# Performance work log

Measured on AMD Instinct MI355X. Metric: run time of the kernel, lower is better.

The kernel has to match this reference:

```python
import jax, jax.numpy as jnp
import numpy as np

D_MODEL, D_HIDDEN, N_EXPERTS, TOP_K = 1024, 2048, 8, 2


def setup_inputs() -> dict:
    key = jax.random.key(0)
    ks = jax.random.split(key, 8)
    s_in = 1.0 / np.sqrt(D_MODEL)
    s_hid = 1.0 / np.sqrt(D_HIDDEN)
    return {
        "x": jax.random.normal(ks[0], (1, 2048, D_MODEL), dtype=jnp.float32),
        # stacked expert weights, stored (in, out) so y = x @ W + b
        "W1": jax.random.normal(ks[1], (N_EXPERTS, D_MODEL, D_HIDDEN), dtype=jnp.float32) * s_in,
        "b1": jnp.zeros((N_EXPERTS, D_HIDDEN), dtype=jnp.float32),
        "W2": jax.random.normal(ks[2], (N_EXPERTS, D_MODEL, D_HIDDEN), dtype=jnp.float32) * s_in,
        "b2": jnp.zeros((N_EXPERTS, D_HIDDEN), dtype=jnp.float32),
        "Wo": jax.random.normal(ks[3], (N_EXPERTS, D_HIDDEN, D_MODEL), dtype=jnp.float32) * s_hid,
        "bo": jnp.zeros((N_EXPERTS, D_MODEL), dtype=jnp.float32),
        "Wr": jax.random.normal(ks[4], (D_MODEL, N_EXPERTS), dtype=jnp.float32) * s_in,
        "br": jnp.zeros((N_EXPERTS,), dtype=jnp.float32),
    }


def reference(x, W1, b1, W2, b2, Wo, bo, Wr, br):
    B, S, D = x.shape
    T = B * S
    xf = x.reshape(T, D)

    # router
    logits = xf @ Wr + br                      # [T, E]
    probs = jax.nn.softmax(logits, axis=-1)
    topk_probs, topk_idx = jax.lax.top_k(probs, TOP_K)  # [T, K]

    # combine weights: c[t, e] = sum_k topk_probs[t, k] * 1[topk_idx[t, k] == e]
    c = jnp.zeros((T, N_EXPERTS), dtype=xf.dtype)
    c = c.at[jnp.arange(T)[:, None], topk_idx].add(topk_probs)  # [T, E]

    # per-expert SwiGLU FFN applied densely, then masked-combined (same math
    # as the original gather/scatter loop since c[t,e]=0 for unrouted experts)
    h = jnp.einsum('td,edh->eth', xf, W1) + b1[:, None, :]   # [E, T, H]
    g = jnp.einsum('td,edh->eth', xf, W2) + b2[:, None, :]
    y = jnp.einsum('eth,ehd->etd', h * jax.nn.silu(g), Wo) + bo[:, None, :]
    out = jnp.einsum('etd,te->td', y, c).reshape(B, S, D)

    probs_mean = probs.mean(axis=0)
    lb_loss = (probs_mean * probs_mean).sum() * N_EXPERTS
    return out, lb_loss
```

## Files before the change

kernel.cpp:

```cpp
#include <hip/hip_runtime.h>
#include <hip/hip_bf16.h>

#define T_TOK 2048
#define DM 1024
#define DH 2048
#define NE 8
#define MT_MAX 40

using bf16x8 = __attribute__((ext_vector_type(8))) short;
using f32x4  = __attribute__((ext_vector_type(4))) float;

__device__ __forceinline__ unsigned short f2bf(float f) {
  union { float f; unsigned u; } v; v.f = f;
  unsigned r = v.u + 0x7FFFu + ((v.u >> 16) & 1u);
  return (unsigned short)(r >> 16);
}
__device__ __forceinline__ unsigned pk2(float a, float b) {
  return (unsigned)f2bf(a) | ((unsigned)f2bf(b) << 16);
}

#define GLOAD16(gsrc, ldst)                                                        \
  __builtin_amdgcn_global_load_lds(                                                \
      (const __attribute__((address_space(1))) unsigned int*)(gsrc),               \
      (__attribute__((address_space(3))) unsigned int*)(ldst), 16, 0, 0)

__global__ __launch_bounds__(256) void k_router(
    const float* __restrict__ x, const float* __restrict__ Wr, const float* __restrict__ br,
    int* __restrict__ cnt, int* __restrict__ idx, float* __restrict__ wgt,
    int* __restrict__ t2r, float* __restrict__ probs, unsigned short* __restrict__ xb)
{
  const int wave = threadIdx.x >> 6, l = threadIdx.x & 63;
  const int t = blockIdx.x * 4 + wave;
  float xv[16];
#pragma unroll
  for (int i = 0; i < 16; ++i) xv[i] = x[t*DM + l + 64*i];
#pragma unroll
  for (int i = 0; i < 16; ++i) xb[t*DM + l + 64*i] = f2bf(xv[i]);

  float acc[8] = {0.f,0.f,0.f,0.f,0.f,0.f,0.f,0.f};
#pragma unroll
  for (int i = 0; i < 16; ++i) {
    const float4* wp = (const float4*)&Wr[(size_t)(l + 64*i)*NE];
    float4 wa = wp[0], wb = wp[1];
    acc[0] += xv[i]*wa.x; acc[1] += xv[i]*wa.y; acc[2] += xv[i]*wa.z; acc[3] += xv[i]*wa.w;
    acc[4] += xv[i]*wb.x; acc[5] += xv[i]*wb.y; acc[6] += xv[i]*wb.z; acc[7] += xv[i]*wb.w;
  }
#pragma unroll
  for (int e = 0; e < 8; ++e) {
#pragma unroll
    for (int off = 32; off; off >>= 1) acc[e] += __shfl_xor(acc[e], off, 64);
    acc[e] += br[e];
  }
  float mx = acc[0];
#pragma unroll
  for (int e = 1; e < 8; ++e) mx = fmaxf(mx, acc[e]);
  float p[8], s = 0.f;
#pragma unroll
  for (int e = 0; e < 8; ++e) { p[e] = expf(acc[e] - mx); s += p[e]; }
  float inv = 1.f / s;
#pragma unroll
  for (int e = 0; e < 8; ++e) p[e] *= inv;

  int e0 = 0; float p0 = p[0];
#pragma unroll
  for (int e = 1; e < 8; ++e) if (p[e] > p0) { p0 = p[e]; e0 = e; }
  int e1 = -1; float p1 = -1.f;
#pragma unroll
  for (int e = 0; e < 8; ++e) { if (e == e0) continue; if (p[e] > p1) { p1 = p[e]; e1 = e; } }

  if (l == 0) {
#pragma unroll
    for (int e = 0; e < 8; ++e) probs[t*NE + e] = p[e];
    int pos0 = atomicAdd(&cnt[e0], 1);
    idx[e0*T_TOK + pos0] = t; wgt[e0*T_TOK + pos0] = p0;
    t2r[t*2 + 0] = e0*T_TOK + pos0;
    int pos1 = atomicAdd(&cnt[e1], 1);
    idx[e1*T_TOK + pos1] = t; wgt[e1*T_TOK + pos1] = p1;
    t2r[t*2 + 1] = e1*T_TOK + pos1;
  }
}

__global__ __launch_bounds__(256) void k_finalize(
    const int* __restrict__ cnt, int* __restrict__ rb,
    const float* __restrict__ probs, float* __restrict__ out,
    int* __restrict__ MTp, int* __restrict__ mtab)
{
  __shared__ float red[8][256];
  const int tid = threadIdx.x;
  float s[8] = {0.f,0.f,0.f,0.f,0.f,0.f,0.f,0.f};
  for (int t = tid; t < T_TOK; t += 256) {
#pragma unroll
    for (int e = 0; e < 8; ++e) s[e] += probs[t*NE + e];
  }
#pragma unroll
  for (int e = 0; e < 8; ++e) red[e][tid] = s[e];
  __syncthreads();
  for (int w = 128; w > 0; w >>= 1) {
    if (tid < w) {
#pragma unroll
      for (int e = 0; e < 8; ++e) red[e][tid] += red[e][tid + w];
    }
    __syncthreads();
  }
  if (tid == 0) {
    float lb = 0.f;
#pragma unroll
    for (int e = 0; e < 8; ++e) {
      float mean = red[e][0] * (1.f / T_TOK);
      lb += mean * mean;
    }
    out[2097152] = lb * NE;
    int r = 0, mc = 0;
#pragma unroll
    for (int e = 0; e < 8; ++e) {
      rb[e] = r; r += cnt[e];
      int nmt = (cnt[e] + 127) / 128;
      for (int j = 0; j < nmt; ++j) mtab[mc++] = (e << 16) | j;
    }
    *MTp = mc;
  }
}

__global__ __launch_bounds__(256) void k_convT(
    const float* __restrict__ in, unsigned short* __restrict__ outT,
    int R, int C, int nnt)
{
  const int e = blockIdx.z;
  const int r0 = blockIdx.y * 64, c0 = blockIdx.x * 64;
  __shared__ float t[64][65];
  const int tid = threadIdx.x;
  const int lr = tid >> 4, lc = (tid & 15) * 4;
#pragma unroll
  for (int i = 0; i < 4; ++i) {
    float4 v = *(const float4*)&in[((size_t)e*R + r0 + lr + i*16)*C + c0 + lc];
    t[lr + i*16][lc+0] = v.x; t[lr + i*16][lc+1] = v.y;
    t[lr + i*16][lc+2] = v.z; t[lr + i*16][lc+3] = v.w;
  }
  __syncthreads();
  const int oc = tid >> 3;
  const int od = (tid & 7) * 8;
  const size_t base2 = ((size_t)e*128 + (size_t)(r0 >> 6)*nnt + (c0 >> 8)) * 16384
                     + (size_t)(c0 & 255) * 64;
#pragma unroll
  for (int i = 0; i < 2; ++i) {
    int c = oc + i*32;
    uint4 v;
    v.x = pk2(t[od+0][c], t[od+1][c]);
    v.y = pk2(t[od+2][c], t[od+3][c]);
    v.z = pk2(t[od+4][c], t[od+5][c]);
    v.w = pk2(t[od+6][c], t[od+7][c]);
    *(uint4*)&outT[base2 + (size_t)c*64 + od] = v;
  }
}

#define TM1 128
#define TN1 64
#define BKK 64

__global__ __launch_bounds__(256) void k_ffn1b(
    const unsigned short* __restrict__ xb,
    const unsigned short* __restrict__ W1T, const float* __restrict__ b1,
    const unsigned short* __restrict__ W2T, const float* __restrict__ b2,
    const int* __restrict__ cnt, const int* __restrict__ rbp,
    const int* __restrict__ idx, unsigned short* __restrict__ act,
    const int* __restrict__ MTp, const int* __restrict__ mtab)
{
  const int mtg = blockIdx.y;
  if (mtg >= *MTp) return;
  const int code = mtab[mtg];
  const int e = code >> 16, mt = code & 0xffff;
  const int Me = cnt[e];
  const int m0 = mt * TM1;
  const int nt = blockIdx.x;
  const int n0 = nt * TN1;

  __shared__ __align__(16) unsigned short As[TM1*BKK];
  __shared__ __align__(16) unsigned short Bh[TN1*BKK];
  __shared__ __align__(16) unsigned short Bg[TN1*BKK];
  __shared__ int toks[TM1];

  const int tid = threadIdx.x;
  if (tid < TM1) toks[tid] = idx[e*T_TOK + min(m0 + tid, Me - 1)];
  __syncthreads();

  const int lane = tid & 63;
  const int wave = tid >> 6;
  const int wm = wave >> 1, wn = wave & 1;
  const int row16 = lane & 15, kg = lane >> 4;
  const int sl = lane & 7;
  const int lr = lane >> 3;

  const unsigned short* asrc[4];
#pragma unroll
  for (int i = 0; i < 4; ++i) {
    int r = (wave*4 + i)*8 + lr;
    asrc[i] = &xb[(size_t)toks[r]*DM + ((sl ^ (r & 7)) * 8)];
  }
  const unsigned short *bsrc1[2], *bsrc2[2];
  const int nt256 = n0 >> 8, nsub = n0 & 255;
#pragma unroll
  for (int j = 0; j < 2; ++j) {
    int r = (wave*2 + j)*8 + lr;
    size_t gb = ((size_t)e*128 + nt256)*16384 + (size_t)(nsub + r)*64 + ((sl ^ (r & 7)) * 8);
    bsrc1[j] = &W1T[gb]; bsrc2[j] = &W2T[gb];
  }

  f32x4 ah[4][2], ag[4][2];
#pragma unroll
  for (int i = 0; i < 4; ++i)
#pragma unroll
    for (int j = 0; j < 2; ++j) { ah[i][j] = 0.f; ag[i][j] = 0.f; }

  for (int k0 = 0; k0 < DM; k0 += BKK) {
    const size_t bko = (size_t)k0 * 2048;
#pragma unroll
    for (int i = 0; i < 4; ++i)
      GLOAD16(asrc[i] + k0, &As[(wave*4 + i)*512]);
#pragma unroll
    for (int j = 0; j < 2; ++j) {
      GLOAD16(bsrc1[j] + bko, &Bh[(wave*2 + j)*512]);
      GLOAD16(bsrc2[j] + bko, &Bg[(wave*2 + j)*512]);
    }
    __syncthreads();
#pragma unroll
    for (int ks = 0; ks < 2; ++ks) {
      const int kslot = ks*4 + kg;
      bf16x8 a[4], vbh[2], vbg[2];
#pragma unroll
      for (int mi = 0; mi < 4; ++mi) {
        int m = wm*64 + mi*16 + row16;
        a[mi] = *(const bf16x8*)&As[m*BKK + ((kslot ^ (m & 7)) * 8)];
      }
#pragma unroll
      for (int ni = 0; ni < 2; ++ni) {
        int n = wn*32 + ni*16 + row16;
        int off = n*BKK + ((kslot ^ (n & 7)) * 8);
        vbh[ni] = *(const bf16x8*)&Bh[off];
        vbg[ni] = *(const bf16x8*)&Bg[off];
      }
#pragma unroll
      for (int mi = 0; mi < 4; ++mi)
#pragma unroll
        for (int ni = 0; ni < 2; ++ni) {
          ah[mi][ni] = __builtin_amdgcn_mfma_f32_16x16x32_bf16(a[mi], vbh[ni], ah[mi][ni], 0, 0, 0);
          ag[mi][ni] = __builtin_amdgcn_mfma_f32_16x16x32_bf16(a[mi], vbg[ni], ag[mi][ni], 0, 0, 0);
        }
    }
    __syncthreads();
  }

  const int rb = rbp[e];
#pragma unroll
  for (int mi = 0; mi < 4; ++mi) {
#pragma unroll
    for (int i = 0; i < 4; ++i) {
      int rloc = wm*64 + mi*16 + (lane >> 4)*4 + i;
      int m = m0 + rloc;
      if (m < Me) {
#pragma unroll
        for (int ni = 0; ni < 2; ++ni) {
          int col = n0 + wn*32 + ni*16 + row16;
          float h = ah[mi][ni][i] + b1[e*DH + col];
          float g = ag[mi][ni][i] + b2[e*DH + col];
          float sg = g / (1.f + __expf(-g));
          act[(size_t)(rb + m)*DH + col] = f2bf(h * sg);
        }
      }
    }
  }
}

__global__ __launch_bounds__(256) void k_ffn2b(
    const unsigned short* __restrict__ act,
    const unsigned short* __restrict__ WoT, const float* __restrict__ bo,
    const int* __restrict__ cnt, const int* __restrict__ rbp,
    const int* __restrict__ idx, const float* __restrict__ wgt,
    float* __restrict__ out,
    const int* __restrict__ MTp, const int* __restrict__ mtab)
{
  const int mtg = blockIdx.y;
  if (mtg >= *MTp) return;
  const int code = mtab[mtg];
  const int e = code >> 16, mt = code & 0xffff;
  const int Me = cnt[e];
  const int m0 = mt * TM1;
  const int nt = blockIdx.x;
  const int n0 = nt * TN1;
  const int rb = rbp[e];

  __shared__ __align__(16) unsigned short As[TM1*BKK];
  __shared__ __align__(16) unsigned short Bs[TN1*BKK];
  __shared__ int   toks[TM1];
  __shared__ float wgts[TM1];

  const int tid = threadIdx.x;
  if (tid < TM1) {
    int p = min(m0 + tid, Me - 1);
    toks[tid] = idx[e*T_TOK + p];
    wgts[tid] = wgt[e*T_TOK + p];
  }

  const int lane = tid & 63;
  const int wave = tid >> 6;
  const int wm = wave >> 1, wn = wave & 1;
  const int row16 = lane & 15, kg = lane >> 4;
  const int sl = lane & 7;
  const int lr = lane >> 3;

  const unsigned short* asrc[4];
#pragma unroll
  for (int i = 0; i < 4; ++i) {
    int r = (wave*4 + i)*8 + lr;
    int grow = rb + min(m0 + r, Me - 1);
    asrc[i] = &act[(size_t)grow*DH + ((sl ^ (r & 7)) * 8)];
  }
  const unsigned short* bsrc[2];
  const int nt256 = n0 >> 8, nsub = n0 & 255;
#pragma unroll
  for (int j = 0; j < 2; ++j) {
    int r = (wave*2 + j)*8 + lr;
    size_t gb = ((size_t)e*128 + nt256)*16384 + (size_t)(nsub + r)*64 + ((sl ^ (r & 7)) * 8);
    bsrc[j] = &WoT[gb];
  }

  f32x4 acc[4][2];
#pragma unroll
  for (int i = 0; i < 4; ++i)
#pragma unroll
    for (int j = 0; j < 2; ++j) acc[i][j] = 0.f;

  for (int k0 = 0; k0 < DH; k0 += BKK) {
    const size_t bko = (size_t)k0 * 1024;
#pragma unroll
    for (int i = 0; i < 4; ++i)
      GLOAD16(asrc[i] + k0, &As[(wave*4 + i)*512]);
#pragma unroll
    for (int j = 0; j < 2; ++j)
      GLOAD16(bsrc[j] + bko, &Bs[(wave*2 + j)*512]);
    __syncthreads();
#pragma unroll
    for (int ks = 0; ks < 2; ++ks) {
      const int kslot = ks*4 + kg;
      bf16x8 a[4], b[2];
#pragma unroll
      for (int mi = 0; mi < 4; ++mi) {
        int m = wm*64 + mi*16 + row16;
        a[mi] = *(const bf16x8*)&As[m*BKK + ((kslot ^ (m & 7)) * 8)];
      }
#pragma unroll
      for (int ni = 0; ni < 2; ++ni) {
        int n = wn*32 + ni*16 + row16;
        b[ni] = *(const bf16x8*)&Bs[n*BKK + ((kslot ^ (n & 7)) * 8)];
      }
#pragma unroll
      for (int mi = 0; mi < 4; ++mi)
#pragma unroll
        for (int ni = 0; ni < 2; ++ni)
          acc[mi][ni] = __builtin_amdgcn_mfma_f32_16x16x32_bf16(a[mi], b[ni], acc[mi][ni], 0, 0, 0);
    }
    __syncthreads();
  }

#pragma unroll
  for (int mi = 0; mi < 4; ++mi) {
#pragma unroll
    for (int i = 0; i < 4; ++i) {
      int rloc = wm*64 + mi*16 + (lane >> 4)*4 + i;
      int m = m0 + rloc;
      if (m < Me) {
        const int t = toks[rloc];
        const float w = wgts[rloc];
#pragma unroll
        for (int ni = 0; ni < 2; ++ni) {
          int col = n0 + wn*32 + ni*16 + row16;
          float y = acc[mi][ni][i] + bo[e*DM + col];
          atomicAdd(&out[(size_t)t*DM + col], w * y);
        }
      }
    }
  }
}

extern "C" void kernel_launch(void* const* d_in, const int* in_sizes, int n_in,
                              void* d_out, int out_size, void* d_ws, size_t ws_size,
                              hipStream_t stream)
{
  const float* x  = (const float*)d_in[0];
  const float* W1 = (const float*)d_in[1];
  const float* b1 = (const float*)d_in[2];
  const float* W2 = (const float*)d_in[3];
  const float* b2 = (const float*)d_in[4];
  const float* Wo = (const float*)d_in[5];
  const float* bo = (const float*)d_in[6];
  const float* Wr = (const float*)d_in[7];
  const float* br = (const float*)d_in[8];
  float* out = (float*)d_out;

  char* ws = (char*)d_ws;
  int*   cnt   = (int*)(ws + 0);
  int*   rb    = (int*)(ws + 64);
  int*   MTp   = (int*)(ws + 128);
  int*   mtab  = (int*)(ws + 192);
  int*   t2r   = (int*)(ws + 4096);
  int*   idx   = (int*)(ws + 32*1024);
  float* wgt   = (float*)(ws + 96*1024);
  float* probs = (float*)(ws + 160*1024);
  unsigned short* xb  = (unsigned short*)(ws + 256*1024);
  unsigned short* act = (unsigned short*)(ws + 5ull*1024*1024);
  unsigned short* W1T = (unsigned short*)(ws + 40ull*1024*1024);
  unsigned short* W2T = (unsigned short*)(ws + 72ull*1024*1024);
  unsigned short* WoT = (unsigned short*)(ws + 104ull*1024*1024);

  hipMemsetAsync(out, 0, (size_t)out_size * sizeof(float), stream);
  hipMemsetAsync(cnt, 0, NE * sizeof(int), stream);
  k_router<<<T_TOK/4, 256, 0, stream>>>(x, Wr, br, cnt, idx, wgt, t2r, probs, xb);
  k_finalize<<<1, 256, 0, stream>>>(cnt, rb, probs, out, MTp, mtab);
  k_convT<<<dim3(DH/64, DM/64, NE), 256, 0, stream>>>(W1, W1T, DM, DH, 8);
  k_convT<<<dim3(DH/64, DM/64, NE), 256, 0, stream>>>(W2, W2T, DM, DH, 8);
  k_convT<<<dim3(DM/64, DH/64, NE), 256, 0, stream>>>(Wo, WoT, DH, DM, 4);
  k_ffn1b<<<dim3(DH/TN1, MT_MAX), 256, 0, stream>>>(xb, W1T, b1, W2T, b2, cnt, rb, idx, act, MTp, mtab);
  k_ffn2b<<<dim3(DM/TN1, MT_MAX), 256, 0, stream>>>(act, WoT, bo, cnt, rb, idx, wgt, out, MTp, mtab);
}
```

Before: 223.5 us.

## Fuse router with weight conversion kernels and widen ffn2 N tile

```diff
diff --git a/kernel.cpp b/kernel.cpp
--- a/kernel.cpp
+++ b/kernel.cpp
@@ -24,59 +24,99 @@
       (const __attribute__((address_space(1))) unsigned int*)(gsrc),               \
       (__attribute__((address_space(3))) unsigned int*)(ldst), 16, 0, 0)
 
-__global__ __launch_bounds__(256) void k_router(
+__global__ __launch_bounds__(256) void k_rconv(
     const float* __restrict__ x, const float* __restrict__ Wr, const float* __restrict__ br,
     int* __restrict__ cnt, int* __restrict__ idx, float* __restrict__ wgt,
-    int* __restrict__ t2r, float* __restrict__ probs, unsigned short* __restrict__ xb)
+    float* __restrict__ probs, unsigned short* __restrict__ xb,
+    const float* __restrict__ W1, const float* __restrict__ W2, const float* __restrict__ Wo,
+    unsigned short* __restrict__ W1T, unsigned short* __restrict__ W2T,
+    unsigned short* __restrict__ WoT)
 {
-  const int wave = threadIdx.x >> 6, l = threadIdx.x & 63;
-  const int t = blockIdx.x * 4 + wave;
-  float xv[16];
-#pragma unroll
-  for (int i = 0; i < 16; ++i) xv[i] = x[t*DM + l + 64*i];
-#pragma unroll
-  for (int i = 0; i < 16; ++i) xb[t*DM + l + 64*i] = f2bf(xv[i]);
-
-  float acc[8] = {0.f,0.f,0.f,0.f,0.f,0.f,0.f,0.f};
-#pragma unroll
-  for (int i = 0; i < 16; ++i) {
-    const float4* wp = (const float4*)&Wr[(size_t)(l + 64*i)*NE];
-    float4 wa = wp[0], wb = wp[1];
-    acc[0] += xv[i]*wa.x; acc[1] += xv[i]*wa.y; acc[2] += xv[i]*wa.z; acc[3] += xv[i]*wa.w;
-    acc[4] += xv[i]*wb.x; acc[5] += xv[i]*wb.y; acc[6] += xv[i]*wb.z; acc[7] += xv[i]*wb.w;
-  }
-#pragma unroll
-  for (int e = 0; e < 8; ++e) {
-#pragma unroll
-    for (int off = 32; off; off >>= 1) acc[e] += __shfl_xor(acc[e], off, 64);
-    acc[e] += br[e];
-  }
-  float mx = acc[0];
-#pragma unroll
-  for (int e = 1; e < 8; ++e) mx = fmaxf(mx, acc[e]);
-  float p[8], s = 0.f;
-#pragma unroll
-  for (int e = 0; e < 8; ++e) { p[e] = expf(acc[e] - mx); s += p[e]; }
-  float inv = 1.f / s;
-#pragma unroll
-  for (int e = 0; e < 8; ++e) p[e] *= inv;
-
-  int e0 = 0; float p0 = p[0];
-#pragma unroll
-  for (int e = 1; e < 8; ++e) if (p[e] > p0) { p0 = p[e]; e0 = e; }
-  int e1 = -1; float p1 = -1.f;
-#pragma unroll
-  for (int e = 0; e < 8; ++e) { if (e == e0) continue; if (p[e] > p1) { p1 = p[e]; e1 = e; } }
-
-  if (l == 0) {
-#pragma unroll
-    for (int e = 0; e < 8; ++e) probs[t*NE + e] = p[e];
-    int pos0 = atomicAdd(&cnt[e0], 1);
-    idx[e0*T_TOK + pos0] = t; wgt[e0*T_TOK + pos0] = p0;
-    t2r[t*2 + 0] = e0*T_TOK + pos0;
-    int pos1 = atomicAdd(&cnt[e1], 1);
-    idx[e1*T_TOK + pos1] = t; wgt[e1*T_TOK + pos1] = p1;
-    t2r[t*2 + 1] = e1*T_TOK + pos1;
+  __shared__ float ts[64][65];
+  const int tid = threadIdx.x;
+
+  if (blockIdx.x < 512) {
+    const int wave = tid >> 6, l = tid & 63;
+    const int t = blockIdx.x * 4 + wave;
+    float xv[16];
+#pragma unroll
+    for (int i = 0; i < 16; ++i) xv[i] = x[t*DM + l + 64*i];
+#pragma unroll
+    for (int i = 0; i < 16; ++i) xb[t*DM + l + 64*i] = f2bf(xv[i]);
+
+    float acc[8] = {0.f,0.f,0.f,0.f,0.f,0.f,0.f,0.f};
+#pragma unroll
+    for (int i = 0; i < 16; ++i) {
+      const float4* wp = (const float4*)&Wr[(size_t)(l + 64*i)*NE];
+      float4 wa = wp[0], wb = wp[1];
+      acc[0] += xv[i]*wa.x; acc[1] += xv[i]*wa.y; acc[2] += xv[i]*wa.z; acc[3] += xv[i]*wa.w;
+      acc[4] += xv[i]*wb.x; acc[5] += xv[i]*wb.y; acc[6] += xv[i]*wb.z; acc[7] += xv[i]*wb.w;
+    }
+#pragma unroll
+    for (int e = 0; e < 8; ++e) {
+#pragma unroll
+      for (int off = 32; off; off >>= 1) acc[e] += __shfl_xor(acc[e], off, 64);
+      acc[e] += br[e];
+    }
+    float mx = acc[0];
+#pragma unroll
+    for (int e = 1; e < 8; ++e) mx = fmaxf(mx, acc[e]);
+    float p[8], s = 0.f;
+#pragma unroll
+    for (int e = 0; e < 8; ++e) { p[e] = expf(acc[e] - mx); s += p[e]; }
+    float inv = 1.f / s;
+#pragma unroll
+    for (int e = 0; e < 8; ++e) p[e] *= inv;
+
+    int e0 = 0; float p0 = p[0];
+#pragma unroll
+    for (int e = 1; e < 8; ++e) if (p[e] > p0) { p0 = p[e]; e0 = e; }
+    int e1 = -1; float p1 = -1.f;
+#pragma unroll
+    for (int e = 0; e < 8; ++e) { if (e == e0) continue; if (p[e] > p1) { p1 = p[e]; e1 = e; } }
+
+    if (l == 0) {
+#pragma unroll
+      for (int e = 0; e < 8; ++e) probs[t*NE + e] = p[e];
+      int pos0 = atomicAdd(&cnt[e0], 1);
+      idx[e0*T_TOK + pos0] = t; wgt[e0*T_TOK + pos0] = p0;
+      int pos1 = atomicAdd(&cnt[e1], 1);
+      idx[e1*T_TOK + pos1] = t; wgt[e1*T_TOK + pos1] = p1;
+    }
+    return;
+  }
+
+  int b = blockIdx.x - 512;
+  const float* in; unsigned short* outT; int R, C, nnt, csh;
+  if (b < 4096)      { in = W1; outT = W1T; R = DM; C = DH; nnt = 8; csh = 5; }
+  else if (b < 8192) { in = W2; outT = W2T; R = DM; C = DH; nnt = 8; csh = 5; b -= 4096; }
+  else               { in = Wo; outT = WoT; R = DH; C = DM; nnt = 4; csh = 4; b -= 8192; }
+  const int e  = b >> 9;
+  const int te = b & 511;
+  const int r0 = (te >> csh) << 6;
+  const int c0 = (te & ((1 << csh) - 1)) << 6;
+
+  const int lr = tid >> 4, lc = (tid & 15) * 4;
+#pragma unroll
+  for (int i = 0; i < 4; ++i) {
+    float4 v = *(const float4*)&in[((size_t)e*R + r0 + lr + i*16)*C + c0 + lc];
+    ts[lr + i*16][lc+0] = v.x; ts[lr + i*16][lc+1] = v.y;
+    ts[lr + i*16][lc+2] = v.z; ts[lr + i*16][lc+3] = v.w;
+  }
+  __syncthreads();
+  const int oc = tid >> 3;
+  const int od = (tid & 7) * 8;
+  const size_t base2 = ((size_t)e*128 + (size_t)(r0 >> 6)*nnt + (c0 >> 8)) * 16384
+                     + (size_t)(c0 & 255) * 64;
+#pragma unroll
+  for (int i = 0; i < 2; ++i) {
+    int c = oc + i*32;
+    uint4 v;
+    v.x = pk2(ts[od+0][c], ts[od+1][c]);
+    v.y = pk2(ts[od+2][c], ts[od+3][c]);
+    v.z = pk2(ts[od+4][c], ts[od+5][c]);
+    v.w = pk2(ts[od+6][c], ts[od+7][c]);
+    *(uint4*)&outT[base2 + (size_t)c*64 + od] = v;
   }
 }
 
@@ -118,38 +158,6 @@
       for (int j = 0; j < nmt; ++j) mtab[mc++] = (e << 16) | j;
     }
     *MTp = mc;
-  }
-}
-
-__global__ __launch_bounds__(256) void k_convT(
-    const float* __restrict__ in, unsigned short* __restrict__ outT,
-    int R, int C, int nnt)
-{
-  const int e = blockIdx.z;
-  const int r0 = blockIdx.y * 64, c0 = blockIdx.x * 64;
-  __shared__ float t[64][65];
-  const int tid = threadIdx.x;
-  const int lr = tid >> 4, lc = (tid & 15) * 4;
-#pragma unroll
-  for (int i = 0; i < 4; ++i) {
-    float4 v = *(const float4*)&in[((size_t)e*R + r0 + lr + i*16)*C + c0 + lc];
-    t[lr + i*16][lc+0] = v.x; t[lr + i*16][lc+1] = v.y;
-    t[lr + i*16][lc+2] = v.z; t[lr + i*16][lc+3] = v.w;
-  }
-  __syncthreads();
-  const int oc = tid >> 3;
-  const int od = (tid & 7) * 8;
-  const size_t base2 = ((size_t)e*128 + (size_t)(r0 >> 6)*nnt + (c0 >> 8)) * 16384
-                     + (size_t)(c0 & 255) * 64;
-#pragma unroll
-  for (int i = 0; i < 2; ++i) {
-    int c = oc + i*32;
-    uint4 v;
-    v.x = pk2(t[od+0][c], t[od+1][c]);
-    v.y = pk2(t[od+2][c], t[od+3][c]);
-    v.z = pk2(t[od+4][c], t[od+5][c]);
-    v.w = pk2(t[od+6][c], t[od+7][c]);
-    *(uint4*)&outT[base2 + (size_t)c*64 + od] = v;
   }
 }
 
@@ -270,6 +278,8 @@
   }
 }
 
+#define TN2 128
+
 __global__ __launch_bounds__(256) void k_ffn2b(
     const unsigned short* __restrict__ act,
     const unsigned short* __restrict__ WoT, const float* __restrict__ bo,
@@ -285,11 +295,11 @@
   const int Me = cnt[e];
   const int m0 = mt * TM1;
   const int nt = blockIdx.x;
-  const int n0 = nt * TN1;
+  const int n0 = nt * TN2;
   const int rb = rbp[e];
 
   __shared__ __align__(16) unsigned short As[TM1*BKK];
-  __shared__ __align__(16) unsigned short Bs[TN1*BKK];
+  __shared__ __align__(16) unsigned short Bs[TN2*BKK];
   __shared__ int   toks[TM1];
   __shared__ float wgts[TM1];
 
@@ -314,20 +324,20 @@
     int grow = rb + min(m0 + r, Me - 1);
     asrc[i] = &act[(size_t)grow*DH + ((sl ^ (r & 7)) * 8)];
   }
-  const unsigned short* bsrc[2];
+  const unsigned short* bsrc[4];
   const int nt256 = n0 >> 8, nsub = n0 & 255;
 #pragma unroll
-  for (int j = 0; j < 2; ++j) {
-    int r = (wave*2 + j)*8 + lr;
+  for (int j = 0; j < 4; ++j) {
+    int r = (wave*4 + j)*8 + lr;
     size_t gb = ((size_t)e*128 + nt256)*16384 + (size_t)(nsub + r)*64 + ((sl ^ (r & 7)) * 8);
     bsrc[j] = &WoT[gb];
   }
 
-  f32x4 acc[4][2];
+  f32x4 acc[4][4];
 #pragma unroll
   for (int i = 0; i < 4; ++i)
 #pragma unroll
-    for (int j = 0; j < 2; ++j) acc[i][j] = 0.f;
+    for (int j = 0; j < 4; ++j) acc[i][j] = 0.f;
 
   for (int k0 = 0; k0 < DH; k0 += BKK) {
     const size_t bko = (size_t)k0 * 1024;
@@ -335,27 +345,27 @@
     for (int i = 0; i < 4; ++i)
       GLOAD16(asrc[i] + k0, &As[(wave*4 + i)*512]);
 #pragma unroll
-    for (int j = 0; j < 2; ++j)
-      GLOAD16(bsrc[j] + bko, &Bs[(wave*2 + j)*512]);
+    for (int j = 0; j < 4; ++j)
+      GLOAD16(bsrc[j] + bko, &Bs[(wave*4 + j)*512]);
     __syncthreads();
 #pragma unroll
     for (int ks = 0; ks < 2; ++ks) {
       const int kslot = ks*4 + kg;
-      bf16x8 a[4], b[2];
+      bf16x8 a[4], b[4];
 #pragma unroll
       for (int mi = 0; mi < 4; ++mi) {
         int m = wm*64 + mi*16 + row16;
         a[mi] = *(const bf16x8*)&As[m*BKK + ((kslot ^ (m & 7)) * 8)];
       }
 #pragma unroll
-      for (int ni = 0; ni < 2; ++ni) {
-        int n = wn*32 + ni*16 + row16;
+      for (int ni = 0; ni < 4; ++ni) {
+        int n = wn*64 + ni*16 + row16;
         b[ni] = *(const bf16x8*)&Bs[n*BKK + ((kslot ^ (n & 7)) * 8)];
       }
 #pragma unroll
       for (int mi = 0; mi < 4; ++mi)
 #pragma unroll
-        for (int ni = 0; ni < 2; ++ni)
+        for (int ni = 0; ni < 4; ++ni)
           acc[mi][ni] = __builtin_amdgcn_mfma_f32_16x16x32_bf16(a[mi], b[ni], acc[mi][ni], 0, 0, 0);
     }
     __syncthreads();
@@ -371,8 +381,8 @@
         const int t = toks[rloc];
         const float w = wgts[rloc];
 #pragma unroll
-        for (int ni = 0; ni < 2; ++ni) {
-          int col = n0 + wn*32 + ni*16 + row16;
+        for (int ni = 0; ni < 4; ++ni) {
+          int col = n0 + wn*64 + ni*16 + row16;
           float y = acc[mi][ni][i] + bo[e*DM + col];
           atomicAdd(&out[(size_t)t*DM + col], w * y);
         }
@@ -401,7 +411,6 @@
   int*   rb    = (int*)(ws + 64);
   int*   MTp   = (int*)(ws + 128);
   int*   mtab  = (int*)(ws + 192);
-  int*   t2r   = (int*)(ws + 4096);
   int*   idx   = (int*)(ws + 32*1024);
   float* wgt   = (float*)(ws + 96*1024);
   float* probs = (float*)(ws + 160*1024);
@@ -413,11 +422,9 @@
 
   hipMemsetAsync(out, 0, (size_t)out_size * sizeof(float), stream);
   hipMemsetAsync(cnt, 0, NE * sizeof(int), stream);
-  k_router<<<T_TOK/4, 256, 0, stream>>>(x, Wr, br, cnt, idx, wgt, t2r, probs, xb);
+  k_rconv<<<512 + 12288, 256, 0, stream>>>(x, Wr, br, cnt, idx, wgt, probs, xb,
+                                           W1, W2, Wo, W1T, W2T, WoT);
   k_finalize<<<1, 256, 0, stream>>>(cnt, rb, probs, out, MTp, mtab);
-  k_convT<<<dim3(DH/64, DM/64, NE), 256, 0, stream>>>(W1, W1T, DM, DH, 8);
-  k_convT<<<dim3(DH/64, DM/64, NE), 256, 0, stream>>>(W2, W2T, DM, DH, 8);
-  k_convT<<<dim3(DM/64, DH/64, NE), 256, 0, stream>>>(Wo, WoT, DH, DM, 4);
   k_ffn1b<<<dim3(DH/TN1, MT_MAX), 256, 0, stream>>>(xb, W1T, b1, W2T, b2, cnt, rb, idx, act, MTp, mtab);
-  k_ffn2b<<<dim3(DM/TN1, MT_MAX), 256, 0, stream>>>(act, WoT, bo, cnt, rb, idx, wgt, out, MTp, mtab);
-}
+  k_ffn2b<<<dim3(DM/TN2, MT_MAX), 256, 0, stream>>>(act, WoT, bo, cnt, rb, idx, wgt, out, MTp, mtab);
+}
```

Result: no change. 226.6 us (+1.4%).
